# Kernel optimization log

Measured on AMD Instinct MI355X. Metric: run time of the kernel, lower is better.

Reference implementation:

```python
import jax, jax.numpy as jnp
import numpy as np

N_HEADS = 8
HIDDEN = 256
D_HEAD = HIDDEN // N_HEADS
N_NODES = 4096
N_EDGES = 16384


def setup_inputs() -> dict:
    key = jax.random.key(0)
    ks = jax.random.split(key, 12)
    s = 0.05
    return {
        "q": jax.random.normal(ks[0], (N_EDGES, HIDDEN), jnp.float32),
        "k": jax.random.normal(ks[1], (N_NODES, HIDDEN), jnp.float32),
        "v": jax.random.normal(ks[2], (N_NODES, HIDDEN), jnp.float32),
        "T": jax.random.uniform(ks[3], (N_NODES, N_EDGES), jnp.float32),
        "Wq": jax.random.normal(ks[4], (HIDDEN, HIDDEN), jnp.float32) * s,
        "bq": jax.random.normal(ks[5], (HIDDEN,), jnp.float32) * s,
        "Wk": jax.random.normal(ks[6], (HIDDEN, HIDDEN), jnp.float32) * s,
        "bk": jax.random.normal(ks[7], (HIDDEN,), jnp.float32) * s,
        "Wv": jax.random.normal(ks[8], (HIDDEN, HIDDEN), jnp.float32) * s,
        "bv": jax.random.normal(ks[9], (HIDDEN,), jnp.float32) * s,
        "Wo": jax.random.normal(ks[10], (HIDDEN, HIDDEN), jnp.float32) * s,
        "bo": jax.random.normal(ks[11], (HIDDEN,), jnp.float32) * s,
    }


def reference(q, k, v, T, Wq, bq, Wk, bk, Wv, bv, Wo, bo):
    scale = D_HEAD ** (-0.5)
    # projections, reshaped to per-head layout
    qh = (q @ Wq.T + bq).reshape(-1, N_HEADS, D_HEAD)  # [E, H, d]
    kh = (k @ Wk.T + bk).reshape(-1, N_HEADS, D_HEAD)  # [N, H, d]
    vh = (v @ Wv.T + bv).reshape(-1, N_HEADS, D_HEAD)  # [N, H, d]
    # row-normalized transition matrix (rows with zero sum left unscaled)
    row_sum = jnp.sum(T, axis=-1, keepdims=True)       # [N, 1]
    Tn = T / jnp.where(row_sum == 0, 1.0, row_sum)     # [N, E]
    # edge->node aggregation of queries, then scale
    qn = jnp.einsum("ne,ehd->nhd", Tn, qh) * scale     # [N, H, d]
    # attention: full NxN scores per head
    scores = jnp.einsum("nhd,mhd->hnm", qn, kh)        # [H, N, N]
    attn = jax.nn.softmax(scores, axis=-1)
    ctx = jnp.einsum("hnm,mhd->nhd", attn, vh)         # [N, H, d]
    out = ctx.reshape(-1, N_HEADS * D_HEAD) @ Wo.T + bo  # [N, hidden]
    return out
```

## Files before the change

### kernel.cpp

```cpp
#include <hip/hip_runtime.h>


#define N_NODES 4096
#define N_EDGES 16384
#define HIDDEN  256
#define KSPLIT  16

typedef __attribute__((ext_vector_type(4))) float f32x4;
typedef __attribute__((ext_vector_type(8))) short s16x8;
typedef __attribute__((ext_vector_type(4))) unsigned short u16x4;
typedef __attribute__((ext_vector_type(8))) unsigned short u16x8;

__device__ __forceinline__ unsigned short f2bf(float f) {
    union { float f; unsigned u; } x; x.f = f;
    unsigned r = x.u + 0x7FFFu + ((x.u >> 16) & 1u);
    return (unsigned short)(r >> 16);
}
__device__ __forceinline__ s16x8 pack8s(f32x4 x, f32x4 y) {
    u16x8 o;
    o[0]=f2bf(x[0]); o[1]=f2bf(x[1]); o[2]=f2bf(x[2]); o[3]=f2bf(x[3]);
    o[4]=f2bf(y[0]); o[5]=f2bf(y[1]); o[6]=f2bf(y[2]); o[7]=f2bf(y[3]);
    union { u16x8 u; s16x8 s; } c; c.u = o; return c.s;
}

__global__ __launch_bounds__(256)
void cvtW(const float* __restrict__ Wq, const float* __restrict__ Wk,
          const float* __restrict__ Wv, const float* __restrict__ Wo,
          unsigned short* __restrict__ dst)
{
    const int g = blockIdx.x * 256 + threadIdx.x;
    const long base = (long)g * 8;
    const int mat = (int)(base >> 16), off = (int)(base & 65535);
    const float* src = (mat == 0) ? Wq : (mat == 1) ? Wk : (mat == 2) ? Wv : Wo;
    f32x4 x = *(const f32x4*)&src[off];
    f32x4 y = *(const f32x4*)&src[off + 4];
    union { u16x8 u; s16x8 s; } c; c.s = pack8s(x, y);
    *(u16x8*)&dst[base] = c.u;
}

template<int MODE>
__global__ __launch_bounds__(256)
void proj_mfma(const float* __restrict__ A, const unsigned short* __restrict__ Wbf,
               const float* __restrict__ bias, unsigned short* __restrict__ out, int M)
{
    const int t = threadIdx.x;
    const int w = t >> 6, l = t & 63, lo = l & 15, h4 = l >> 4;
    const int m0 = blockIdx.x * 64 + w * 16;
    const int bn = blockIdx.y * 64;
    const float* Ar = A + (long)(m0 + lo) * 256 + h4 * 8;

    f32x4 acc[4] = {};
    #pragma unroll
    for (int kk = 0; kk < 8; ++kk) {
        f32x4 x = *(const f32x4*)&Ar[kk * 32];
        f32x4 y = *(const f32x4*)&Ar[kk * 32 + 4];
        s16x8 af = pack8s(x, y);
        #pragma unroll
        for (int nj = 0; nj < 4; ++nj) {
            s16x8 bf = *(const s16x8*)&Wbf[(bn + nj * 16 + lo) * 256 + kk * 32 + h4 * 8];
            acc[nj] = __builtin_amdgcn_mfma_f32_16x16x32_bf16(af, bf, acc[nj], 0, 0, 0);
        }
    }
    #pragma unroll
    for (int nj = 0; nj < 4; ++nj) {
        const int n = bn + nj * 16 + lo;
        const float bi = bias[n];
        if (MODE == 1) {
            #pragma unroll
            for (int r = 0; r < 4; ++r)
                out[(long)(m0 + h4 * 4 + r) * 256 + n] = f2bf(acc[nj][r] + bi);
        } else {
            u16x4 o;
            #pragma unroll
            for (int r = 0; r < 4; ++r) o[r] = f2bf(acc[nj][r] + bi);
            *(u16x4*)&out[(long)n * M + m0 + h4 * 4] = o;
        }
    }
}

__global__ __launch_bounds__(256)
void proj_out_mfma(const float* __restrict__ pctx, const float* __restrict__ plp,
                   const unsigned short* __restrict__ Wobf, const float* __restrict__ bo,
                   float* __restrict__ out)
{
    const int t = threadIdx.x;
    const int w = t >> 6, l = t & 63, lo = l & 15, h4 = l >> 4;
    const int m0 = blockIdx.x * 64 + w * 16;
    const int bn = blockIdx.y * 64;
    const int m = m0 + lo;

    float inv[8];
    #pragma unroll
    for (int h = 0; h < 8; ++h) {
        float s = plp[(0 * 8 + h) * N_NODES + m] + plp[(1 * 8 + h) * N_NODES + m]
                + plp[(2 * 8 + h) * N_NODES + m] + plp[(3 * 8 + h) * N_NODES + m];
        inv[h] = 1.0f / s;
    }
    const float* P = pctx + (long)m * 256;
    const long PS = (long)N_NODES * 256;

    f32x4 acc[4] = {};
    #pragma unroll
    for (int kk = 0; kk < 8; ++kk) {
        const int off = kk * 32 + h4 * 8;
        f32x4 x = *(const f32x4*)&P[off]          + *(const f32x4*)&P[PS + off]
                + *(const f32x4*)&P[2 * PS + off] + *(const f32x4*)&P[3 * PS + off];
        f32x4 y = *(const f32x4*)&P[off + 4]          + *(const f32x4*)&P[PS + off + 4]
                + *(const f32x4*)&P[2 * PS + off + 4] + *(const f32x4*)&P[3 * PS + off + 4];
        s16x8 af = pack8s(x * inv[kk], y * inv[kk]);
        #pragma unroll
        for (int nj = 0; nj < 4; ++nj) {
            s16x8 bf = *(const s16x8*)&Wobf[(bn + nj * 16 + lo) * 256 + kk * 32 + h4 * 8];
            acc[nj] = __builtin_amdgcn_mfma_f32_16x16x32_bf16(af, bf, acc[nj], 0, 0, 0);
        }
    }
    #pragma unroll
    for (int nj = 0; nj < 4; ++nj) {
        const int n = bn + nj * 16 + lo;
        const float bi = bo[n];
        #pragma unroll
        for (int r = 0; r < 4; ++r)
            out[(long)(m0 + h4 * 4 + r) * 256 + n] = acc[nj][r] + bi;
    }
}

__global__ __launch_bounds__(512, 4)
void tgemm(const float* __restrict__ T, const unsigned short* __restrict__ Bt,
           float* __restrict__ part, float* __restrict__ rsp)
{
    __shared__ __align__(16) unsigned short Bsm[2][256 * 64];
    const int t  = threadIdx.x;
    const int ks = blockIdx.x & 15, ms = blockIdx.x >> 4;
    const int m0 = ms * 128;
    const long k00 = (long)ks * 1024;
    const int w = t >> 6, l = t & 63, lo = l & 15, h4 = l >> 4;

    const int kx = ((l & 7) * 8) ^ ((l >> 3) << 3);
    const unsigned short* Bsrc = Bt + k00 + kx;

#define STAGE(itv, bufv) do {                                                       \
    const unsigned short* _s = Bsrc + (long)(itv) * 64;                             \
    unsigned short* _d = &Bsm[(bufv)][w * 2048];                                    \
    _Pragma("unroll")                                                               \
    for (int _i = 0; _i < 4; ++_i)                                                  \
        __builtin_amdgcn_global_load_lds(                                           \
            (const __attribute__((address_space(1))) unsigned int*)                 \
                (_s + (long)(w * 32 + _i * 8 + (l >> 3)) * N_EDGES),                \
            (__attribute__((address_space(3))) unsigned int*)(_d + _i * 512),       \
            16, 0, 0);                                                              \
} while (0)

    const float* Arow = T + (long)(m0 + w * 16 + lo) * N_EDGES + k00 + h4 * 8;

    f32x4 a0 = *(const f32x4*)&Arow[0];
    f32x4 a1 = *(const f32x4*)&Arow[4];
    f32x4 a2 = *(const f32x4*)&Arow[32];
    f32x4 a3 = *(const f32x4*)&Arow[36];
    STAGE(0, 0);

    f32x4 acc[16] = {};
    float rs = 0.f;

    for (int it = 0; it < 16; ++it) {
        const int cur = it & 1;
        __builtin_amdgcn_s_barrier();
        if (it < 15) {
            STAGE(it + 1, cur ^ 1);
            asm volatile("s_waitcnt vmcnt(4)" ::: "memory");
        } else {
            asm volatile("s_waitcnt vmcnt(0)" ::: "memory");
        }
        s16x8 af0 = pack8s(a0, a1);
        s16x8 af1 = pack8s(a2, a3);
        rs += a0[0]+a0[1]+a0[2]+a0[3] + a1[0]+a1[1]+a1[2]+a1[3]
            + a2[0]+a2[1]+a2[2]+a2[3] + a3[0]+a3[1]+a3[2]+a3[3];
        if (it < 15) {
            const float* An = Arow + (it + 1) * 64;
            a0 = *(const f32x4*)&An[0];
            a1 = *(const f32x4*)&An[4];
            a2 = *(const f32x4*)&An[32];
            a3 = *(const f32x4*)&An[36];
        }
        __builtin_amdgcn_s_barrier();
        __builtin_amdgcn_sched_barrier(0);

        const unsigned short* Bb = Bsm[cur];
        const int swz = (lo & 7) << 3;
        #pragma unroll
        for (int nj = 0; nj < 16; ++nj) {
            const int jb = (nj * 16 + lo) * 64;
            s16x8 bf0 = *(const s16x8*)&Bb[jb + ((h4 * 8) ^ swz)];
            s16x8 bf1 = *(const s16x8*)&Bb[jb + ((32 + h4 * 8) ^ swz)];
            acc[nj] = __builtin_amdgcn_mfma_f32_16x16x32_bf16(af0, bf0, acc[nj], 0, 0, 0);
            acc[nj] = __builtin_amdgcn_mfma_f32_16x16x32_bf16(af1, bf1, acc[nj], 0, 0, 0);
        }
    }
#undef STAGE

    rs += __shfl_xor(rs, 16); rs += __shfl_xor(rs, 32);
    if (h4 == 0) rsp[ks * N_NODES + m0 + w * 16 + lo] = rs;

    float* P = part + (long)ks * (N_NODES * HIDDEN);
    #pragma unroll
    for (int nj = 0; nj < 16; ++nj)
        #pragma unroll
        for (int r = 0; r < 4; ++r)
            P[(long)(m0 + w * 16 + h4 * 4 + r) * HIDDEN + nj * 16 + lo] = acc[nj][r];
}

__global__ __launch_bounds__(256)
void finalize(const float* __restrict__ part, const float* __restrict__ rsp,
              unsigned short* __restrict__ qn)
{
    const int idx = blockIdx.x * 256 + threadIdx.x;
    const long i4 = (long)idx * 4;
    const int n = (int)(i4 >> 8);
    f32x4 s = {};
    #pragma unroll
    for (int ksp = 0; ksp < KSPLIT; ++ksp)
        s += *(const f32x4*)&part[(long)ksp * (N_NODES * HIDDEN) + i4];
    float rs = 0.f;
    #pragma unroll
    for (int ksp = 0; ksp < KSPLIT; ++ksp) rs += rsp[ksp * N_NODES + n];
    rs = (rs == 0.0f) ? 1.0f : rs;
    const float sc = 0.17677669529663687f / rs;
    u16x4 o;
    #pragma unroll
    for (int i = 0; i < 4; ++i) o[i] = f2bf(s[i] * sc);
    *(u16x4*)&qn[i4] = o;
}

__global__ __launch_bounds__(256)
void attn(const unsigned short* __restrict__ qn, const unsigned short* __restrict__ kh,
          const unsigned short* __restrict__ vht, float* __restrict__ pctx,
          float* __restrict__ plp)
{
    __shared__ __align__(16) unsigned short Ksm[64 * 40];
    __shared__ __align__(16) unsigned short Vsm[32 * 72];
    __shared__ __align__(16) unsigned short Psm[4][32 * 72];
    const int t  = threadIdx.x;
    const int hh = blockIdx.x >> 7, nb = (blockIdx.x >> 2) & 31, mh = blockIdx.x & 3;
    const int w = t >> 6, l = t & 63, lo = l & 15, h4 = l >> 4;
    const int n0 = nb * 128 + w * 32;

    const int km = t >> 2, kdc = (t & 3) * 8;
    const int vd = t >> 3, vmc = (t & 7) * 8;

    s16x8 qf[2];
    #pragma unroll
    for (int ni = 0; ni < 2; ++ni)
        qf[ni] = *(const s16x8*)&qn[(long)(n0 + ni * 16 + lo) * HIDDEN + hh * 32 + h4 * 8];

    f32x4 acc[2][2] = {};
    float lp[2][4] = {};
    const f32x4 zero = {};

    for (int mt = mh * 16; mt < mh * 16 + 16; ++mt) {
        const int m0 = mt * 64;
        *(s16x8*)&Ksm[km * 40 + kdc] =
            *(const s16x8*)&kh[(long)(m0 + km) * HIDDEN + hh * 32 + kdc];
        *(s16x8*)&Vsm[vd * 72 + vmc] =
            *(const s16x8*)&vht[(long)(hh * 32 + vd) * N_NODES + m0 + vmc];
        __syncthreads();

        s16x8 kb[4];
        #pragma unroll
        for (int mi = 0; mi < 4; ++mi)
            kb[mi] = *(const s16x8*)&Ksm[(mi * 16 + lo) * 40 + h4 * 8];
        #pragma unroll
        for (int ni = 0; ni < 2; ++ni) {
            #pragma unroll
            for (int mi = 0; mi < 4; ++mi) {
                f32x4 s = __builtin_amdgcn_mfma_f32_16x16x32_bf16(qf[ni], kb[mi], zero, 0, 0, 0);
                #pragma unroll
                for (int r = 0; r < 4; ++r) {
                    float p = __expf(s[r]);
                    lp[ni][r] += p;
                    Psm[w][(ni * 16 + h4 * 4 + r) * 72 + mi * 16 + lo] = f2bf(p);
                }
            }
        }
        s16x8 pa[2][2], vb[2][2];
        #pragma unroll
        for (int ni = 0; ni < 2; ++ni)
            #pragma unroll
            for (int k2 = 0; k2 < 2; ++k2)
                pa[ni][k2] = *(const s16x8*)&Psm[w][(ni * 16 + lo) * 72 + k2 * 32 + h4 * 8];
        #pragma unroll
        for (int di = 0; di < 2; ++di)
            #pragma unroll
            for (int k2 = 0; k2 < 2; ++k2)
                vb[di][k2] = *(const s16x8*)&Vsm[(di * 16 + lo) * 72 + k2 * 32 + h4 * 8];
        #pragma unroll
        for (int k2 = 0; k2 < 2; ++k2)
            #pragma unroll
            for (int ni = 0; ni < 2; ++ni)
                #pragma unroll
                for (int di = 0; di < 2; ++di)
                    acc[ni][di] = __builtin_amdgcn_mfma_f32_16x16x32_bf16(
                        pa[ni][k2], vb[di][k2], acc[ni][di], 0, 0, 0);
        __syncthreads();
    }
    #pragma unroll
    for (int ni = 0; ni < 2; ++ni)
        #pragma unroll
        for (int r = 0; r < 4; ++r) {
            float v2 = lp[ni][r];
            v2 += __shfl_xor(v2, 1); v2 += __shfl_xor(v2, 2);
            v2 += __shfl_xor(v2, 4); v2 += __shfl_xor(v2, 8);
            lp[ni][r] = v2;
        }
    float* myctx = pctx + (long)mh * (N_NODES * HIDDEN);
    float* myplp = plp  + (long)(mh * 8 + hh) * N_NODES;
    if (lo == 0)
        #pragma unroll
        for (int ni = 0; ni < 2; ++ni)
            #pragma unroll
            for (int r = 0; r < 4; ++r)
                myplp[n0 + ni * 16 + h4 * 4 + r] = lp[ni][r];
    #pragma unroll
    for (int ni = 0; ni < 2; ++ni)
        #pragma unroll
        for (int di = 0; di < 2; ++di)
            #pragma unroll
            for (int r = 0; r < 4; ++r)
                myctx[(long)(n0 + ni * 16 + h4 * 4 + r) * HIDDEN + hh * 32 + di * 16 + lo]
                    = acc[ni][di][r];
}

extern "C" void kernel_launch(void* const* d_in, const int* in_sizes, int n_in,
                              void* d_out, int out_size, void* d_ws, size_t ws_size,
                              hipStream_t stream)
{
    const float* q  = (const float*)d_in[0];
    const float* k  = (const float*)d_in[1];
    const float* v  = (const float*)d_in[2];
    const float* T  = (const float*)d_in[3];
    const float* Wq = (const float*)d_in[4];  const float* bq = (const float*)d_in[5];
    const float* Wk = (const float*)d_in[6];  const float* bk = (const float*)d_in[7];
    const float* Wv = (const float*)d_in[8];  const float* bv = (const float*)d_in[9];
    const float* Wo = (const float*)d_in[10]; const float* bo = (const float*)d_in[11];

    char* w = (char*)d_ws;
    unsigned short* qh_t = (unsigned short*)(w);
    unsigned short* kh   = (unsigned short*)(w + (8u  << 20));
    unsigned short* vh_t = (unsigned short*)(w + (10u << 20));
    unsigned short* qn   = (unsigned short*)(w + (12u << 20));
    float*          pctx = (float*)         (w + (14u << 20));
    float*          plp  = (float*)         (w + (30u << 20));
    float*          part = (float*)         (w + (32u << 20));
    float*          rsp  = (float*)         (w + (96u << 20));
    unsigned short* wbf  = (unsigned short*)(w + (97u << 20));
    unsigned short* wq_bf = wbf;
    unsigned short* wk_bf = wbf + 65536;
    unsigned short* wv_bf = wbf + 2 * 65536;
    unsigned short* wo_bf = wbf + 3 * 65536;

    cvtW<<<128, 256, 0, stream>>>(Wq, Wk, Wv, Wo, wbf);
    proj_mfma<2><<<dim3(256, 4), 256, 0, stream>>>(q, wq_bf, bq, qh_t, N_EDGES);
    proj_mfma<1><<<dim3(64, 4),  256, 0, stream>>>(k, wk_bf, bk, kh,   N_NODES);
    proj_mfma<2><<<dim3(64, 4),  256, 0, stream>>>(v, wv_bf, bv, vh_t, N_NODES);
    tgemm<<<512, 512, 0, stream>>>(T, qh_t, part, rsp);
    finalize<<<1024, 256, 0, stream>>>(part, rsp, qn);
    attn<<<1024, 256, 0, stream>>>(qn, kh, vh_t, pctx, plp);
    proj_out_mfma<<<dim3(64, 4), 256, 0, stream>>>(pctx, plp, wo_bf, bo, (float*)d_out);
}
```

Measured before the change: 213.1 us.

## Split attention key range 8 ways and prefetch K/V tiles into registers

The attention kernel now splits the key dimension into 8 chunks instead of 4, which doubles the grid to 2048 blocks for more parallelism and occupancy. Workspace buffers for partial contexts and log-sum partials are enlarged to hold 8 partials, and the output projection now reduces 8 partials. The K/V global loads for the next tile are issued into registers right after the barrier so they overlap with the current tile's MFMA work. The cost is twice the partial-context traffic written by attn and read back by the output projection.

Result: slower. 217.9 us (+2.3%).

```diff
diff --git a/kernel.cpp b/kernel.cpp
--- a/kernel.cpp
+++ b/kernel.cpp
@@ -92,8 +92,9 @@
     float inv[8];
     #pragma unroll
     for (int h = 0; h < 8; ++h) {
-        float s = plp[(0 * 8 + h) * N_NODES + m] + plp[(1 * 8 + h) * N_NODES + m]
-                + plp[(2 * 8 + h) * N_NODES + m] + plp[(3 * 8 + h) * N_NODES + m];
+        float s = 0.f;
+        #pragma unroll
+        for (int p = 0; p < 8; ++p) s += plp[(p * 8 + h) * N_NODES + m];
         inv[h] = 1.0f / s;
     }
     const float* P = pctx + (long)m * 256;
@@ -103,10 +104,12 @@
     #pragma unroll
     for (int kk = 0; kk < 8; ++kk) {
         const int off = kk * 32 + h4 * 8;
-        f32x4 x = *(const f32x4*)&P[off]          + *(const f32x4*)&P[PS + off]
-                + *(const f32x4*)&P[2 * PS + off] + *(const f32x4*)&P[3 * PS + off];
-        f32x4 y = *(const f32x4*)&P[off + 4]          + *(const f32x4*)&P[PS + off + 4]
-                + *(const f32x4*)&P[2 * PS + off + 4] + *(const f32x4*)&P[3 * PS + off + 4];
+        f32x4 x = {}, y = {};
+        #pragma unroll
+        for (int p = 0; p < 8; ++p) {
+            x += *(const f32x4*)&P[p * PS + off];
+            y += *(const f32x4*)&P[p * PS + off + 4];
+        }
         s16x8 af = pack8s(x * inv[kk], y * inv[kk]);
         #pragma unroll
         for (int nj = 0; nj < 4; ++nj) {
@@ -239,7 +242,7 @@
     __shared__ __align__(16) unsigned short Vsm[32 * 72];
     __shared__ __align__(16) unsigned short Psm[4][32 * 72];
     const int t  = threadIdx.x;
-    const int hh = blockIdx.x >> 7, nb = (blockIdx.x >> 2) & 31, mh = blockIdx.x & 3;
+    const int hh = blockIdx.x >> 8, nb = (blockIdx.x >> 3) & 31, mh = blockIdx.x & 7;
     const int w = t >> 6, l = t & 63, lo = l & 15, h4 = l >> 4;
     const int n0 = nb * 128 + w * 32;
 
@@ -250,18 +253,24 @@
     #pragma unroll
     for (int ni = 0; ni < 2; ++ni)
         qf[ni] = *(const s16x8*)&qn[(long)(n0 + ni * 16 + lo) * HIDDEN + hh * 32 + h4 * 8];
+
+    const unsigned short* kp = &kh[(long)(mh * 512 + km) * HIDDEN + hh * 32 + kdc];
+    const unsigned short* vp = &vht[(long)(hh * 32 + vd) * N_NODES + mh * 512 + vmc];
+    s16x8 kreg = *(const s16x8*)kp;
+    s16x8 vreg = *(const s16x8*)vp;
 
     f32x4 acc[2][2] = {};
     float lp[2][4] = {};
     const f32x4 zero = {};
 
-    for (int mt = mh * 16; mt < mh * 16 + 16; ++mt) {
-        const int m0 = mt * 64;
-        *(s16x8*)&Ksm[km * 40 + kdc] =
-            *(const s16x8*)&kh[(long)(m0 + km) * HIDDEN + hh * 32 + kdc];
-        *(s16x8*)&Vsm[vd * 72 + vmc] =
-            *(const s16x8*)&vht[(long)(hh * 32 + vd) * N_NODES + m0 + vmc];
+    for (int it = 0; it < 8; ++it) {
+        *(s16x8*)&Ksm[km * 40 + kdc] = kreg;
+        *(s16x8*)&Vsm[vd * 72 + vmc] = vreg;
         __syncthreads();
+        if (it < 7) {
+            kreg = *(const s16x8*)(kp + (long)(it + 1) * 64 * HIDDEN);
+            vreg = *(const s16x8*)(vp + (it + 1) * 64);
+        }
 
         s16x8 kb[4];
         #pragma unroll
@@ -347,10 +356,10 @@
     unsigned short* vh_t = (unsigned short*)(w + (10u << 20));
     unsigned short* qn   = (unsigned short*)(w + (12u << 20));
     float*          pctx = (float*)         (w + (14u << 20));
-    float*          plp  = (float*)         (w + (30u << 20));
-    float*          part = (float*)         (w + (32u << 20));
-    float*          rsp  = (float*)         (w + (96u << 20));
-    unsigned short* wbf  = (unsigned short*)(w + (97u << 20));
+    float*          plp  = (float*)         (w + (46u << 20));
+    float*          part = (float*)         (w + (48u << 20));
+    float*          rsp  = (float*)         (w + (112u << 20));
+    unsigned short* wbf  = (unsigned short*)(w + (113u << 20));
     unsigned short* wq_bf = wbf;
     unsigned short* wk_bf = wbf + 65536;
     unsigned short* wv_bf = wbf + 2 * 65536;
@@ -362,6 +371,6 @@
     proj_mfma<2><<<dim3(64, 4),  256, 0, stream>>>(v, wv_bf, bv, vh_t, N_NODES);
     tgemm<<<512, 512, 0, stream>>>(T, qh_t, part, rsp);
     finalize<<<1024, 256, 0, stream>>>(part, rsp, qn);
-    attn<<<1024, 256, 0, stream>>>(qn, kh, vh_t, pctx, plp);
+    attn<<<2048, 256, 0, stream>>>(qn, kh, vh_t, pctx, plp);
     proj_out_mfma<<<dim3(64, 4), 256, 0, stream>>>(pctx, plp, wo_bf, bo, (float*)d_out);
 }
```
